# Kernel optimization log

Hardware: AMD Instinct MI355X
Metric: run time of the kernel (lower is better)

## Reference

```python
import jax, jax.numpy as jnp
import numpy as np

# Architecture constants (match init_kwargs)
SHAPES = [(128, 128), (64, 64), (32, 32), (16, 16)]  # (H, W) per level
L, P, NH, D, DH = 4, 4, 8, 256, 32
NLAYERS, DFFN, BS = 6, 1024, 2
N = sum(h * w for h, w in SHAPES)  # 21760


def setup_inputs() -> dict:
    key = jax.random.key(0)
    ks = iter(jax.random.split(key, 64))
    def nrm(shape, s=0.02):
        return s * jax.random.normal(next(ks), shape, jnp.float32)
    inp = {}
    for i, (h, w) in enumerate(SHAPES):
        inp[f"src{i}"] = jax.random.normal(next(ks), (BS, D, h, w), jnp.float32)
        inp[f"pos{i}"] = 0.1 * jax.random.normal(next(ks), (BS, D, h, w), jnp.float32)
    inp["level_embed"] = nrm((L, D), 1.0)
    inp["W_off"] = nrm((NLAYERS, NH * L * P * 2, D)); inp["b_off"] = nrm((NLAYERS, NH * L * P * 2), 0.5)
    inp["W_attn"] = nrm((NLAYERS, NH * L * P, D)); inp["b_attn"] = jnp.zeros((NLAYERS, NH * L * P), jnp.float32)
    inp["W_val"] = nrm((NLAYERS, D, D)); inp["b_val"] = jnp.zeros((NLAYERS, D), jnp.float32)
    inp["W_out"] = nrm((NLAYERS, D, D)); inp["b_out"] = jnp.zeros((NLAYERS, D), jnp.float32)
    inp["g_na"] = jnp.ones((NLAYERS, D), jnp.float32); inp["g_nf"] = jnp.ones((NLAYERS, D), jnp.float32)
    inp["ls_a"] = jnp.full((NLAYERS, D), 1e-4, jnp.float32); inp["ls_f"] = jnp.full((NLAYERS, D), 1e-4, jnp.float32)
    inp["W1"] = nrm((NLAYERS, DFFN, D)); inp["b1"] = jnp.zeros((NLAYERS, DFFN), jnp.float32)
    inp["W3"] = nrm((NLAYERS, DFFN, D)); inp["b3"] = jnp.zeros((NLAYERS, DFFN), jnp.float32)
    inp["W2"] = nrm((NLAYERS, D, DFFN)); inp["b2"] = jnp.zeros((NLAYERS, D), jnp.float32)
    return inp


def rmsnorm(x, g):
    return x * jax.lax.rsqrt(jnp.mean(x * x, axis=-1, keepdims=True) + 1e-6) * g


def reference_points():
    # valid_ratios == 1 (all shapes divisible by 32 -> masks all False), so
    # reference points are identical across levels: [N, 2] in (x, y) normalized.
    refs = []
    for h, w in SHAPES:
        ry = (jnp.arange(h, dtype=jnp.float32) + 0.5) / h
        rx = (jnp.arange(w, dtype=jnp.float32) + 0.5) / w
        gy, gx = jnp.meshgrid(ry, rx, indexing='ij')
        refs.append(jnp.stack([gx.ravel(), gy.ravel()], axis=-1))
    return jnp.concatenate(refs, axis=0)


def deform_sample(value, loc, aw):
    # value: [bs, N, NH, DH]; loc: [bs, Nq, NH, L, P, 2]; aw: [bs, Nq, NH, L, P]
    bs, nq = loc.shape[0], loc.shape[1]
    out = jnp.zeros((bs, NH, nq, DH), jnp.float32)
    start = 0
    for l, (Hl, Wl) in enumerate(SHAPES):
        val = value[:, start:start + Hl * Wl].transpose(0, 2, 1, 3)  # [bs,NH,HW,DH]
        start += Hl * Wl
        # grid_sample(align_corners=False): pixel = loc * size - 0.5, zero padding
        x = loc[:, :, :, l, :, 0] * Wl - 0.5  # [bs,Nq,NH,P]
        y = loc[:, :, :, l, :, 1] * Hl - 0.5
        x0 = jnp.floor(x); y0 = jnp.floor(y)
        acc = jnp.zeros((bs, NH, nq, P, DH), jnp.float32)
        for dx in (0.0, 1.0):
            for dy in (0.0, 1.0):
                xi = x0 + dx; yi = y0 + dy
                w = (1.0 - jnp.abs(x - xi)) * (1.0 - jnp.abs(y - yi))
                valid = (xi >= 0) & (xi < Wl) & (yi >= 0) & (yi < Hl)
                idx = (jnp.clip(yi, 0, Hl - 1) * Wl + jnp.clip(xi, 0, Wl - 1)).astype(jnp.int32)
                idx = idx.transpose(0, 2, 1, 3).reshape(bs, NH, nq * P)
                g = jnp.take_along_axis(val, idx[..., None], axis=2).reshape(bs, NH, nq, P, DH)
                acc = acc + g * (w * valid).transpose(0, 2, 1, 3)[..., None]
        out = out + (acc * aw[:, :, :, l].transpose(0, 2, 1, 3)[..., None]).sum(axis=3)
    return out.transpose(0, 2, 1, 3).reshape(bs, nq, NH * DH)


def msda(q, qpos, ref, Wo, bo, Wa, ba, Wv, bv, Wp, bp):
    # q: pre-normed tokens used both as query and value (identity disabled)
    bs, nq, _ = q.shape
    qin = q + qpos
    value = (q @ Wv.T + bv).reshape(bs, nq, NH, DH)
    off = (qin @ Wo.T + bo).reshape(bs, nq, NH, L, P, 2)
    aw = jax.nn.softmax((qin @ Wa.T + ba).reshape(bs, nq, NH, L * P), axis=-1)
    aw = aw.reshape(bs, nq, NH, L, P)
    normalizer = jnp.array([[w, h] for h, w in SHAPES], jnp.float32)  # [L,2] (x=W,y=H)
    loc = ref[None, :, None, None, None, :] + off / normalizer[None, None, None, :, None, :]
    samp = deform_sample(value, loc, aw)
    return samp @ Wp.T + bp


def reference(src0, src1, src2, src3, pos0, pos1, pos2, pos3, level_embed,
              W_off, b_off, W_attn, b_attn, W_val, b_val, W_out, b_out,
              g_na, g_nf, ls_a, ls_f, W1, b1, W3, b3, W2, b2):
    srcs = [src0, src1, src2, src3]
    poss = [pos0, pos1, pos2, pos3]
    q = jnp.concatenate([s.reshape(BS, D, -1).transpose(0, 2, 1) for s in srcs], axis=1)
    posf = jnp.concatenate(
        [p.reshape(BS, D, -1).transpose(0, 2, 1) + level_embed[i] for i, p in enumerate(poss)], axis=1)
    ref = reference_points()
    for i in range(NLAYERS):
        n = rmsnorm(q, g_na[i])
        a = msda(n, posf, ref, W_off[i], b_off[i], W_attn[i], b_attn[i],
                 W_val[i], b_val[i], W_out[i], b_out[i])
        q = q + ls_a[i] * a
        n = rmsnorm(q, g_nf[i])
        f = (jax.nn.silu(n @ W1[i].T + b1[i]) * (n @ W3[i].T + b3[i])) @ W2[i].T + b2[i]
        q = q + ls_f[i] * f
    spatial_shapes = jnp.array(SHAPES, jnp.int32)
    level_start_index = jnp.concatenate(
        [jnp.zeros((1,), jnp.int32), jnp.cumsum(spatial_shapes.prod(1))[:-1]])
    return q, spatial_shapes, level_start_index
```

## Files before the change

### kernel.cpp

```cpp
#include <hip/hip_runtime.h>

typedef unsigned short u16;
typedef unsigned int   u32;
typedef __bf16 bf16x8 __attribute__((ext_vector_type(8)));
typedef float  f32x4  __attribute__((ext_vector_type(4)));
typedef u16    u16x4  __attribute__((ext_vector_type(4)));
typedef u32    u32x4  __attribute__((ext_vector_type(4)));

#define NTOK 21760
#define TTOK 43520
#define DMODEL 256

__device__ __forceinline__ u16 f2bf(float f){
  u32 u = __builtin_bit_cast(u32, f);
  u32 r = u + 0x7fffu + ((u >> 16) & 1u);
  return (u16)(r >> 16);
}
__device__ __forceinline__ float bf2f(u16 h){
  u32 u = ((u32)h) << 16;
  return __builtin_bit_cast(float, u);
}
__device__ __forceinline__ float lo16(u32 u){ return __builtin_bit_cast(float, u << 16); }
__device__ __forceinline__ float hi16(u32 u){ return __builtin_bit_cast(float, u & 0xffff0000u); }

__device__ __forceinline__ void gld16(const u16* g, u16* l){
  __builtin_amdgcn_global_load_lds((const __attribute__((address_space(1))) void*)g,
                                   (__attribute__((address_space(3))) void*)l, 16, 0, 0);
}

__global__ void cvt_plain(const float* __restrict__ s, u16* __restrict__ d, int n){
  int i = blockIdx.x * 256 + threadIdx.x;
  if (i < n) d[i] = f2bf(s[i]);
}
__global__ void build_oa_w(const float* __restrict__ Wo, const float* __restrict__ Wa, u16* __restrict__ dst){
  int i = blockIdx.x * 256 + threadIdx.x;
  if (i >= 6*384*256) return;
  int l = i / (384*256); int rem = i % (384*256); int r = rem >> 8; int c = rem & 255;
  float v = (r < 256) ? Wo[((size_t)l*256 + r)*256 + c] : Wa[((size_t)l*128 + (r-256))*256 + c];
  dst[i] = f2bf(v);
}
__global__ void build_oa_b(const float* __restrict__ bo, const float* __restrict__ ba, float* __restrict__ dst){
  int i = blockIdx.x * 256 + threadIdx.x;
  if (i >= 6*384) return;
  int l = i / 384; int r = i % 384;
  dst[i] = (r < 256) ? bo[l*256 + r] : ba[l*128 + (r-256)];
}
__global__ void build_w13(const float* __restrict__ W1, const float* __restrict__ W3, u16* __restrict__ dst){
  int i = blockIdx.x * 256 + threadIdx.x;
  if (i >= 6*2048*256) return;
  int l = i / (2048*256); int rem = i % (2048*256); int r = rem >> 8; int c = rem & 255;
  int f = r >> 1; int s = r & 1;
  const float* W = s ? W3 : W1;
  dst[i] = f2bf(W[((size_t)l*1024 + f)*256 + c]);
}
__global__ void build_b13(const float* __restrict__ b1, const float* __restrict__ b3, float* __restrict__ dst){
  int i = blockIdx.x * 256 + threadIdx.x;
  if (i >= 6*2048) return;
  int l = i / 2048; int r = i % 2048;
  dst[i] = (r & 1) ? b3[l*1024 + (r>>1)] : b1[l*1024 + (r>>1)];
}

__global__ __launch_bounds__(256)
void prep_level(const float* __restrict__ src, const float* __restrict__ pos,
                const float* __restrict__ lemb, float* __restrict__ q,
                u16* __restrict__ posf, int HW, int nstart){
  __shared__ float tS[32][65];
  __shared__ float tP[32][65];
  int b  = blockIdx.z;
  int d0 = blockIdx.y * 32;
  int n0 = blockIdx.x * 64;
  int tx = threadIdx.x & 63, ty = threadIdx.x >> 6;
  #pragma unroll
  for (int i = 0; i < 8; ++i){
    int d = i*4 + ty;
    size_t gi = ((size_t)b*DMODEL + d0 + d) * HW + n0 + tx;
    tS[d][tx] = src[gi];
    tP[d][tx] = pos[gi];
  }
  __syncthreads();
  int dc = threadIdx.x & 31, nl0 = threadIdx.x >> 5;
  float le = lemb[d0 + dc];
  #pragma unroll
  for (int ii = 0; ii < 8; ++ii){
    int nl = nl0 + ii*8;
    size_t oi = ((size_t)b*NTOK + nstart + n0 + nl) * DMODEL + d0 + dc;
    q[oi]    = tS[dc][nl];
    posf[oi] = f2bf(tP[dc][nl] + le);
  }
}

__global__ void tail_writer(float* __restrict__ out){
  const float vals[12] = {128.f,128.f,64.f,64.f,32.f,32.f,16.f,16.f,
                          0.f,16384.f,20480.f,21504.f};
  int t = threadIdx.x;
  if (t < 12) out[(size_t)TTOK*DMODEL + t] = vals[t];
}

__global__ __launch_bounds__(256)
void rmsnorm_k(const float* __restrict__ q, const float* __restrict__ g,
               const u16* __restrict__ posf, u16* __restrict__ nout,
               u16* __restrict__ qinout){
  int tok  = blockIdx.x*4 + (threadIdx.x >> 6);
  int lane = threadIdx.x & 63;
  const f32x4* qr = (const f32x4*)(q + (size_t)tok*DMODEL);
  f32x4 v = qr[lane];
  float ss = v[0]*v[0] + v[1]*v[1] + v[2]*v[2] + v[3]*v[3];
  #pragma unroll
  for (int o = 32; o > 0; o >>= 1) ss += __shfl_xor(ss, o);
  float sc = rsqrtf(ss * (1.0f/256.0f) + 1e-6f);
  f32x4 gv = ((const f32x4*)g)[lane];
  float nf[4]; u16x4 nv;
  #pragma unroll
  for (int r = 0; r < 4; ++r){ nf[r] = v[r]*sc*gv[r]; nv[r] = f2bf(nf[r]); }
  ((u16x4*)(nout + (size_t)tok*DMODEL))[lane] = nv;
  if (qinout){
    u16x4 pf = ((const u16x4*)(posf + (size_t)tok*DMODEL))[lane];
    u16x4 qv;
    #pragma unroll
    for (int r = 0; r < 4; ++r) qv[r] = f2bf(nf[r] + bf2f(pf[r]));
    ((u16x4*)(qinout + (size_t)tok*DMODEL))[lane] = qv;
  }
}

template<int EPI>
__global__ __launch_bounds__(256)
void gemm_bt(const u16* __restrict__ A, const u16* __restrict__ B,
             const float* __restrict__ bias, void* __restrict__ outp,
             const float* __restrict__ ls, int K, int ldo){
  __shared__ u16 lds[2][2][4096];
  const int tid = threadIdx.x, lane = tid & 63, w = tid >> 6;
  const int wm = w >> 1, wn = w & 1;
  const int bn = blockIdx.x * 128, bm = blockIdx.y * 128;
  const int fr = lane & 15, ks = lane >> 4;

  const u16* gA = A + (size_t)(bm + w*32 + (lane >> 2)) * K + (lane & 3) * 8;
  const u16* gB = B + (size_t)(bn + w*32 + (lane >> 2)) * K + (lane & 3) * 8;
  const size_t rstep = (size_t)16 * K;

  f32x4 acc[4][4];
  #pragma unroll
  for (int m = 0; m < 4; ++m)
    #pragma unroll
    for (int n = 0; n < 4; ++n) acc[m][n] = (f32x4){0.f,0.f,0.f,0.f};

  const int aoff = (wm*64 + fr)*32 + ks*8;
  const int boff = (wn*64 + fr)*32 + ks*8;

  auto STAGE = [&](int buf, int k0){
    gld16(gA + k0,         &lds[buf][0][w*1024]);
    gld16(gA + k0 + rstep, &lds[buf][0][w*1024 + 512]);
    gld16(gB + k0,         &lds[buf][1][w*1024]);
    gld16(gB + k0 + rstep, &lds[buf][1][w*1024 + 512]);
  };

  const int nk = K >> 5;
  STAGE(0, 0);
  __syncthreads();
  int buf = 0;
  for (int t = 0; t < nk; ++t){
    if (t + 1 < nk) STAGE(buf ^ 1, (t + 1) * 32);
    bf16x8 af[4], bb[4];
    #pragma unroll
    for (int m = 0; m < 4; ++m) af[m] = *(const bf16x8*)&lds[buf][0][aoff + m*512];
    #pragma unroll
    for (int n = 0; n < 4; ++n) bb[n] = *(const bf16x8*)&lds[buf][1][boff + n*512];
    #pragma unroll
    for (int m = 0; m < 4; ++m)
      #pragma unroll
      for (int n = 0; n < 4; ++n)
        acc[m][n] = __builtin_amdgcn_mfma_f32_16x16x32_bf16(af[m], bb[n], acc[m][n], 0, 0, 0);
    __syncthreads();
    buf ^= 1;
  }

  const int colb = bn + wn*64 + fr;
  const int rowb = bm + wm*64 + ks*4;

  if (EPI == 0){
    u16* o = (u16*)outp;
    #pragma unroll
    for (int n = 0; n < 4; ++n){
      int col = colb + n*16; float bv = bias[col];
      #pragma unroll
      for (int m = 0; m < 4; ++m){
        int row = rowb + m*16;
        #pragma unroll
        for (int r = 0; r < 4; ++r)
          o[(size_t)(row + r)*ldo + col] = f2bf(acc[m][n][r] + bv);
      }
    }
  } else if (EPI == 1){
    u16* o = (u16*)outp;
    #pragma unroll
    for (int n = 0; n < 4; ++n){
      int col = colb + n*16; float bv = bias[col];
      int f = col >> 1; bool even = ((col & 1) == 0);
      #pragma unroll
      for (int m = 0; m < 4; ++m){
        int row = rowb + m*16;
        #pragma unroll
        for (int r = 0; r < 4; ++r){
          float v = acc[m][n][r] + bv;
          float other = __shfl_xor(v, 1);
          if (even){
            float res = (v / (1.0f + __expf(-v))) * other;
            o[(size_t)(row + r)*ldo + f] = f2bf(res);
          }
        }
      }
    }
  } else {
    float* o = (float*)outp;
    #pragma unroll
    for (int n = 0; n < 4; ++n){
      int col = colb + n*16; float bv = bias[col]; float lv = ls[col];
      #pragma unroll
      for (int m = 0; m < 4; ++m){
        int row = rowb + m*16;
        #pragma unroll
        for (int r = 0; r < 4; ++r){
          size_t ix = (size_t)(row + r)*ldo + col;
          o[ix] += lv * (acc[m][n][r] + bv);
        }
      }
    }
  }
}

__global__ __launch_bounds__(256)
void sampler_k(const u16* __restrict__ oa, const u16* __restrict__ value,
               u16* __restrict__ samp){
  int t = blockIdx.x * 256 + threadIdx.x;
  int head = t & 7;
  int q = (t >> 3) % NTOK;
  int b = t / (NTOK * 8);

  int lv, st, lw, sh;
  if (q < 16384){ lv = 0; st = 0;     lw = 128; sh = 7; }
  else if (q < 20480){ lv = 1; st = 16384; lw = 64; sh = 6; }
  else if (q < 21504){ lv = 2; st = 20480; lw = 32; sh = 5; }
  else { lv = 3; st = 21504; lw = 16; sh = 4; }
  (void)lv;
  int loc = q - st;
  int j = loc & (lw - 1), i = loc >> sh;
  float invW = 1.0f / (float)lw;
  float rx = (j + 0.5f) * invW, ry = (i + 0.5f) * invW;

  const u16* oq = oa + (size_t)(b*NTOK + q) * 384;
  float lg[16];
  const u32* lg32 = (const u32*)(oq + 256 + head*16);
  #pragma unroll
  for (int p = 0; p < 8; ++p){ u32 wd = lg32[p]; lg[2*p] = lo16(wd); lg[2*p+1] = hi16(wd); }
  float mx = -1e30f;
  #pragma unroll
  for (int p = 0; p < 16; ++p) mx = fmaxf(mx, lg[p]);
  float ssum = 0.f;
  #pragma unroll
  for (int p = 0; p < 16; ++p){ lg[p] = __expf(lg[p] - mx); ssum += lg[p]; }
  float inv = 1.0f / ssum;

  float acc[32];
  #pragma unroll
  for (int d = 0; d < 32; ++d) acc[d] = 0.f;

  const u32* op32 = (const u32*)(oq + head*32);
  int start = 0;
  #pragma unroll
  for (int l = 0; l < 4; ++l){
    const int Wl = 128 >> l;
    #pragma unroll
    for (int p = 0; p < 4; ++p){
      u32 wd = op32[l*4 + p];
      float x = rx * Wl + lo16(wd) - 0.5f;
      float y = ry * Wl + hi16(wd) - 0.5f;
      float x0f = floorf(x), y0f = floorf(y);
      int x0 = (int)x0f, y0 = (int)y0f;
      float fx = x - x0f, fy = y - y0f;
      float wp = lg[l*4 + p];
      #pragma unroll
      for (int c = 0; c < 4; ++c){
        int xi = x0 + (c & 1), yi = y0 + (c >> 1);
        float wc = ((c & 1) ? fx : 1.f - fx) * ((c >> 1) ? fy : 1.f - fy) * wp;
        if (xi >= 0 && xi < Wl && yi >= 0 && yi < Wl && wc != 0.f){
          const u32* vp = (const u32*)(value +
              ((size_t)(b*NTOK + start + yi*Wl + xi) * DMODEL + head*32));
          #pragma unroll
          for (int u = 0; u < 16; ++u){
            u32 uu = vp[u];
            acc[2*u]   += wc * lo16(uu);
            acc[2*u+1] += wc * hi16(uu);
          }
        }
      }
    }
    start += Wl * Wl;
  }
  u16* out = samp + (size_t)(b*NTOK + q) * DMODEL + head*32;
  #pragma unroll
  for (int d = 0; d < 32; d += 4){
    u16x4 o4;
    #pragma unroll
    for (int r = 0; r < 4; ++r) o4[r] = f2bf(acc[d + r] * inv);
    *(u16x4*)(out + d) = o4;
  }
}

extern "C" void kernel_launch(void* const* d_in, const int* in_sizes, int n_in,
                              void* d_out, int out_size, void* d_ws, size_t ws_size,
                              hipStream_t stream){
  const float* src[4] = {(const float*)d_in[0], (const float*)d_in[2],
                         (const float*)d_in[4], (const float*)d_in[6]};
  const float* pos[4] = {(const float*)d_in[1], (const float*)d_in[3],
                         (const float*)d_in[5], (const float*)d_in[7]};
  const float* le     = (const float*)d_in[8];
  const float* W_off  = (const float*)d_in[9];  const float* b_off  = (const float*)d_in[10];
  const float* W_attn = (const float*)d_in[11]; const float* b_attn = (const float*)d_in[12];
  const float* W_val  = (const float*)d_in[13]; const float* b_val  = (const float*)d_in[14];
  const float* W_out  = (const float*)d_in[15]; const float* b_out  = (const float*)d_in[16];
  const float* g_na   = (const float*)d_in[17]; const float* g_nf   = (const float*)d_in[18];
  const float* ls_a   = (const float*)d_in[19]; const float* ls_f   = (const float*)d_in[20];
  const float* W1     = (const float*)d_in[21]; const float* b1     = (const float*)d_in[22];
  const float* W3     = (const float*)d_in[23]; const float* b3     = (const float*)d_in[24];
  const float* W2     = (const float*)d_in[25]; const float* b2     = (const float*)d_in[26];

  char* ws = (char*)d_ws;
  u16*   wv   = (u16*)  (ws + 0);
  u16*   wpj  = (u16*)  (ws + 786432);
  u16*   w2b  = (u16*)  (ws + 1572864);
  u16*   woa  = (u16*)  (ws + 4718592);
  float* boa  = (float*)(ws + 5898240);
  u16*   w13  = (u16*)  (ws + 5907456);
  float* bi13 = (float*)(ws + 12198912);
  u16*   posfb= (u16*)  (ws + 12248064);
  u16*   nb   = (u16*)  (ws + 34530304);
  u16*   qinb = (u16*)  (ws + 56812544);
  u16*   valb = (u16*)  (ws + 79094784);
  u16*   oab  = (u16*)  (ws + 101377024);
  u16*   sampb= (u16*)  (ws + 134800384);
  u16*   hb   = qinb;
  float* qf   = (float*)d_out;

  cvt_plain<<<(393216+255)/256, 256, 0, stream>>>(W_val, wv, 393216);
  cvt_plain<<<(393216+255)/256, 256, 0, stream>>>(W_out, wpj, 393216);
  cvt_plain<<<(1572864+255)/256, 256, 0, stream>>>(W2, w2b, 1572864);
  build_oa_w<<<(589824+255)/256, 256, 0, stream>>>(W_off, W_attn, woa);
  build_oa_b<<<(2304+255)/256, 256, 0, stream>>>(b_off, b_attn, boa);
  build_w13<<<(3145728+255)/256, 256, 0, stream>>>(W1, W3, w13);
  build_b13<<<(12288+255)/256, 256, 0, stream>>>(b1, b3, bi13);

  const int HW[4]  = {16384, 4096, 1024, 256};
  const int nst[4] = {0, 16384, 20480, 21504};
  for (int l = 0; l < 4; ++l){
    dim3 g(HW[l]/64, 8, 2);
    prep_level<<<g, 256, 0, stream>>>(src[l], pos[l], le + l*256, qf, posfb, HW[l], nst[l]);
  }
  tail_writer<<<1, 64, 0, stream>>>(qf);

  for (int l = 0; l < 6; ++l){
    rmsnorm_k<<<10880, 256, 0, stream>>>(qf, g_na + l*256, posfb, nb, qinb);
    gemm_bt<0><<<dim3(3,340), 256, 0, stream>>>(qinb, woa + (size_t)l*98304, boa + l*384, oab, nullptr, 256, 384);
    gemm_bt<0><<<dim3(2,340), 256, 0, stream>>>(nb, wv + (size_t)l*65536, b_val + l*256, valb, nullptr, 256, 256);
    sampler_k<<<1360, 256, 0, stream>>>(oab, valb, sampb);
    gemm_bt<2><<<dim3(2,340), 256, 0, stream>>>(sampb, wpj + (size_t)l*65536, b_out + l*256, qf, ls_a + l*256, 256, 256);
    rmsnorm_k<<<10880, 256, 0, stream>>>(qf, g_nf + l*256, nullptr, nb, nullptr);
    gemm_bt<1><<<dim3(16,340), 256, 0, stream>>>(nb, w13 + (size_t)l*524288, bi13 + l*2048, hb, nullptr, 256, 1024);
    gemm_bt<2><<<dim3(2,340), 256, 0, stream>>>(hb, w2b + (size_t)l*262144, b2 + l*256, qf, ls_f + l*256, 1024, 256);
  }
  (void)in_sizes; (void)n_in; (void)out_size; (void)ws_size;
}
```

Before: 2.561 ms.

## Remap workgroups for XCD locality and split sampler levels across lane pairs

```diff
diff --git a/kernel.cpp b/kernel.cpp
--- a/kernel.cpp
+++ b/kernel.cpp
@@ -130,7 +130,15 @@
   __shared__ u16 lds[2][2][4096];
   const int tid = threadIdx.x, lane = tid & 63, w = tid >> 6;
   const int wm = w >> 1, wn = w & 1;
-  const int bn = blockIdx.x * 128, bm = blockIdx.y * 128;
+
+  const int gx = gridDim.x;
+  const int nwg = gx * gridDim.y;
+  const int id  = blockIdx.y * gx + blockIdx.x;
+  const int q8 = nwg >> 3, r8 = nwg & 7;
+  const int xcd = id & 7, pos = id >> 3;
+  const int nid = (xcd < r8 ? xcd * (q8 + 1) : r8 * (q8 + 1) + (xcd - r8) * q8) + pos;
+  const int bn = (nid % gx) * 128, bm = (nid / gx) * 128;
+
   const int fr = lane & 15, ks = lane >> 4;
 
   const u16* gA = A + (size_t)(bm + w*32 + (lane >> 2)) * K + (lane & 3) * 8;
@@ -230,17 +238,19 @@
 __global__ __launch_bounds__(256)
 void sampler_k(const u16* __restrict__ oa, const u16* __restrict__ value,
                u16* __restrict__ samp){
-  int t = blockIdx.x * 256 + threadIdx.x;
-  int head = t & 7;
-  int q = (t >> 3) % NTOK;
-  int b = t / (NTOK * 8);
-
-  int lv, st, lw, sh;
-  if (q < 16384){ lv = 0; st = 0;     lw = 128; sh = 7; }
-  else if (q < 20480){ lv = 1; st = 16384; lw = 64; sh = 6; }
-  else if (q < 21504){ lv = 2; st = 20480; lw = 32; sh = 5; }
-  else { lv = 3; st = 21504; lw = 16; sh = 4; }
-  (void)lv;
+  int nid = (blockIdx.x & 7) * 340 + (blockIdx.x >> 3);
+  int t = nid * 256 + threadIdx.x;
+  int half = t & 1;
+  int pair = t >> 1;
+  int head = pair & 7;
+  int q = (pair >> 3) % NTOK;
+  int b = pair / (NTOK * 8);
+
+  int st, lw, sh;
+  if (q < 16384){ st = 0;     lw = 128; sh = 7; }
+  else if (q < 20480){ st = 16384; lw = 64; sh = 6; }
+  else if (q < 21504){ st = 20480; lw = 32; sh = 5; }
+  else { st = 21504; lw = 16; sh = 4; }
   int loc = q - st;
   int j = loc & (lw - 1), i = loc >> sh;
   float invW = 1.0f / (float)lw;
@@ -264,10 +274,11 @@
   for (int d = 0; d < 32; ++d) acc[d] = 0.f;
 
   const u32* op32 = (const u32*)(oq + head*32);
-  int start = 0;
-  #pragma unroll
-  for (int l = 0; l < 4; ++l){
-    const int Wl = 128 >> l;
+  #pragma unroll
+  for (int il = 0; il < 2; ++il){
+    const int l = half*2 + il;
+    const int Wl    = il ? (half ? 16 : 64)    : (half ? 32 : 128);
+    const int start = il ? (half ? 21504 : 16384) : (half ? 20480 : 0);
     #pragma unroll
     for (int p = 0; p < 4; ++p){
       u32 wd = op32[l*4 + p];
@@ -282,25 +293,31 @@
         int xi = x0 + (c & 1), yi = y0 + (c >> 1);
         float wc = ((c & 1) ? fx : 1.f - fx) * ((c >> 1) ? fy : 1.f - fy) * wp;
         if (xi >= 0 && xi < Wl && yi >= 0 && yi < Wl && wc != 0.f){
-          const u32* vp = (const u32*)(value +
+          const u32x4* vp = (const u32x4*)(value +
               ((size_t)(b*NTOK + start + yi*Wl + xi) * DMODEL + head*32));
           #pragma unroll
-          for (int u = 0; u < 16; ++u){
-            u32 uu = vp[u];
-            acc[2*u]   += wc * lo16(uu);
-            acc[2*u+1] += wc * hi16(uu);
+          for (int u4 = 0; u4 < 4; ++u4){
+            u32x4 vv = vp[u4];
+            #pragma unroll
+            for (int jj = 0; jj < 4; ++jj){
+              acc[8*u4 + 2*jj]     += wc * lo16(vv[jj]);
+              acc[8*u4 + 2*jj + 1] += wc * hi16(vv[jj]);
+            }
           }
         }
       }
     }
-    start += Wl * Wl;
-  }
-  u16* out = samp + (size_t)(b*NTOK + q) * DMODEL + head*32;
-  #pragma unroll
-  for (int d = 0; d < 32; d += 4){
+  }
+
+  #pragma unroll
+  for (int d = 0; d < 32; ++d) acc[d] += __shfl_xor(acc[d], 1);
+
+  u16* out = samp + (size_t)(b*NTOK + q) * DMODEL + head*32 + half*16;
+  #pragma unroll
+  for (int d = 0; d < 16; d += 4){
     u16x4 o4;
     #pragma unroll
-    for (int r = 0; r < 4; ++r) o4[r] = f2bf(acc[d + r] * inv);
+    for (int r = 0; r < 4; ++r) o4[r] = f2bf(acc[half*16 + d + r] * inv);
     *(u16x4*)(out + d) = o4;
   }
 }
@@ -360,7 +377,7 @@
     rmsnorm_k<<<10880, 256, 0, stream>>>(qf, g_na + l*256, posfb, nb, qinb);
     gemm_bt<0><<<dim3(3,340), 256, 0, stream>>>(qinb, woa + (size_t)l*98304, boa + l*384, oab, nullptr, 256, 384);
     gemm_bt<0><<<dim3(2,340), 256, 0, stream>>>(nb, wv + (size_t)l*65536, b_val + l*256, valb, nullptr, 256, 256);
-    sampler_k<<<1360, 256, 0, stream>>>(oab, valb, sampb);
+    sampler_k<<<2720, 256, 0, stream>>>(oab, valb, sampb);
     gemm_bt<2><<<dim3(2,340), 256, 0, stream>>>(sampb, wpj + (size_t)l*65536, b_out + l*256, qf, ls_a + l*256, 256, 256);
     rmsnorm_k<<<10880, 256, 0, stream>>>(qf, g_nf + l*256, nullptr, nb, nullptr);
     gemm_bt<1><<<dim3(16,340), 256, 0, stream>>>(nb, w13 + (size_t)l*524288, bi13 + l*2048, hb, nullptr, 256, 1024);
```

New measurement: 2.351 ms. -8.2%, faster.
